# Kernel tuning notes

Measured on AMD Instinct MI355X. Metric: run time of the kernel, lower is better.

Reference implementation:

```python
import jax, jax.numpy as jnp
import numpy as np

K = 4  # recurrent_kernel_size


def setup_inputs() -> dict:
    key = jax.random.key(0)
    k1, k2, k3, k4 = jax.random.split(key, 4)
    b, t, d = 4, 4096, 1024
    x = jax.random.normal(k1, (b, t, d), dtype=jnp.float32)
    W_conv = jax.random.normal(k2, (d, 1, K), dtype=jnp.float32) * (1.0 / np.sqrt(K))
    W_proj = jax.random.normal(k3, (4 * d, d), dtype=jnp.float32) * (1.0 / np.sqrt(d))
    W_out = jax.random.normal(k4, (d, d), dtype=jnp.float32) * (1.0 / np.sqrt(d))
    return {"x": x, "W_conv": W_conv, "W_proj": W_proj, "W_out": W_out}


def _causal_dwconv(x_btd, W_conv):
    # x: [b,t,d]; W_conv: [d,1,k] (torch depthwise layout). Causal: left-pad k-1.
    d = x_btd.shape[-1]
    x_bdt = jnp.transpose(x_btd, (0, 2, 1))  # [b,d,t]
    y = jax.lax.conv_general_dilated(
        x_bdt, W_conv,
        window_strides=(1,),
        padding=[(K - 1, 0)],
        feature_group_count=d,
        dimension_numbers=("NCH", "OIH", "NCH"),
    )
    return jnp.transpose(y, (0, 2, 1))  # [b,t,d]


def reference(x, W_conv, W_proj, W_out):
    b, t, d = x.shape
    mixed = _causal_dwconv(x, W_conv)
    u = jnp.einsum("btd,ed->bte", x + mixed, W_proj)  # [b,t,4d]
    v, gate, decay, inject = jnp.split(u, 4, axis=-1)
    gate = jax.nn.sigmoid(gate)
    decay = jax.nn.sigmoid(decay)
    inject = jnp.tanh(inject)

    def step(state, inp):
        dec_t, inj_t, g_t, v_t = inp  # each [b,d]
        state = dec_t * state + (1.0 - dec_t) * inj_t
        out = g_t * v_t + (1.0 - g_t) * state
        return state, out

    # move time to leading axis for scan: [t,b,d]
    seq = (jnp.swapaxes(decay, 0, 1), jnp.swapaxes(inject, 0, 1),
           jnp.swapaxes(gate, 0, 1), jnp.swapaxes(v, 0, 1))
    state0 = jnp.zeros((b, d), dtype=x.dtype)
    _, y_tbd = jax.lax.scan(step, state0, seq)
    y = jnp.swapaxes(y_tbd, 0, 1)  # [b,t,d]
    return jnp.einsum("btd,ed->bte", y, W_out)
```

## Files before the change

kernel.cpp:

```cpp
#include <hip/hip_runtime.h>
#include <hip/hip_bf16.h>
#include <math.h>

typedef __hip_bfloat16 bf16;
typedef __bf16 bf16x8 __attribute__((ext_vector_type(8)));
typedef float f32x4 __attribute__((ext_vector_type(4)));
typedef float f32x4v __attribute__((ext_vector_type(4)));
typedef unsigned short u16x8v __attribute__((ext_vector_type(8)));
typedef unsigned short u16x4v __attribute__((ext_vector_type(4)));

#define BB 4
#define TT 4096
#define DD 1024

__device__ __forceinline__ float fast_sigmoid(float x) {
  return 1.0f / (1.0f + __expf(-x));
}
__device__ __forceinline__ float fast_tanh(float x) {
  return 2.0f / (1.0f + __expf(-2.0f * x)) - 1.0f;
}
__device__ __forceinline__ float b2f(unsigned short u) {
  union { unsigned int i; float f; } x;
  x.i = ((unsigned int)u) << 16;
  return x.f;
}
__device__ __forceinline__ unsigned short f2b(float f) {
  union { bf16 h; unsigned short u; } x;
  x.h = __float2bfloat16(f);
  return x.u;
}

__global__ __launch_bounds__(256) void w2bf_kernel(const float* __restrict__ w,
                                                   bf16* __restrict__ o,
                                                   int n) {
  int i = blockIdx.x * 256 + threadIdx.x;
  if (i < n) o[i] = __float2bfloat16(w[i]);
}

__global__ __launch_bounds__(256) void conv_add_kernel(
    const float* __restrict__ x, const float* __restrict__ Wc,
    bf16* __restrict__ xm, int total4) {
  int i = blockIdx.x * 256 + threadIdx.x;
  if (i >= total4) return;
  int c4 = (i & (DD / 4 - 1)) * 4;
  int t = (i / (DD / 4)) % TT;
  size_t base = (size_t)i * 4;
  f32x4v x0 = *(const f32x4v*)(x + base);
  f32x4v p1 = (t >= 1) ? *(const f32x4v*)(x + base - DD) : (f32x4v)0.0f;
  f32x4v p2 = (t >= 2) ? *(const f32x4v*)(x + base - 2 * DD) : (f32x4v)0.0f;
  f32x4v p3 = (t >= 3) ? *(const f32x4v*)(x + base - 3 * DD) : (f32x4v)0.0f;
  u16x4v o;
#pragma unroll
  for (int j = 0; j < 4; ++j) {
    f32x4v w = *(const f32x4v*)(Wc + (size_t)(c4 + j) * 4);
    float acc = x0[j] + w[3] * x0[j] + w[2] * p1[j] + w[1] * p2[j] +
                w[0] * p3[j];
    o[j] = f2b(acc);
  }
  *(u16x4v*)(xm + base) = o;
}

template <int EP>
__global__ __launch_bounds__(512, 2) void gemm256_kernel(
    const bf16* __restrict__ A, const bf16* __restrict__ B,
    void* __restrict__ C, int M, int N, int K, int MB) {
  __shared__ __align__(16) bf16 As[2][2][128][64];
  __shared__ __align__(16) bf16 Bs[2][2][128][64];

  const int tid = threadIdx.x;
  const int wv = tid >> 6, l = tid & 63;
  const int wm = wv >> 2, wn = wv & 3;

  const int bid = blockIdx.x;
  const int xcd = bid & 7, ii = bid >> 3;
  const int mb8 = MB >> 3;
  const int bm = xcd * mb8 + (ii % mb8);
  const int bn = ii / mb8;
  const int m0 = bm * 256, n0 = bn * 256;

  const int lr3 = l >> 3;
  const int gcolE = ((l & 7) ^ (l >> 3)) * 8;
  const int l15 = l & 15;
  const int rxor = (l15 & 7) << 3;
  const int lhi8 = (l >> 4) * 8;
  const int colK0 = lhi8 ^ rxor;
  const int colK1 = (32 + lhi8) ^ rxor;

  const char* AsB = (const char*)&As[0][0][0][0];
  const char* BsB = (const char*)&Bs[0][0][0][0];
  const int aB0 = wm * 16384 + l15 * 128 + colK0 * 2;
  const int aB1 = wm * 16384 + l15 * 128 + colK1 * 2;
  const int bB0 = (wn >> 1) * 16384 + (wn & 1) * 8192 + l15 * 128 + colK0 * 2;
  const int bB1 = (wn >> 1) * 16384 + (wn & 1) * 8192 + l15 * 128 + colK1 * 2;

  const bf16* Arow = A + (size_t)(m0 + wv * 16 + lr3) * K + gcolE;
  const bf16* Brow = B + (size_t)(n0 + wv * 16 + lr3) * K + gcolE;
  const bf16* ArowH = Arow + (size_t)128 * K;
  const bf16* BrowH = Brow + (size_t)128 * K;

  bf16* AsW = &As[0][0][0][0];
  bf16* BsW = &Bs[0][0][0][0];

  auto stage1 = [&](int which, int k0) {
    const int slot = (k0 >> 6) & 1;
    const bf16* src0 =
        (which == 0 ? Brow : which == 1 ? BrowH : which == 2 ? Arow : ArowH) +
        k0;
    bf16* dst0 = (which < 2 ? BsW : AsW) + slot * 16384 + (which & 1) * 8192 +
                 wv * 1024;
#pragma unroll
    for (int j = 0; j < 2; ++j) {
      __builtin_amdgcn_global_load_lds(
          (const __attribute__((address_space(1))) void*)(src0 +
                                                          (size_t)(j * 8) * K),
          (__attribute__((address_space(3))) void*)(dst0 + j * 512), 16, 0, 0);
    }
  };

  f32x4 acc[8][4];
#pragma unroll
  for (int i = 0; i < 8; ++i)
#pragma unroll
    for (int j = 0; j < 4; ++j) acc[i][j] = (f32x4)0.0f;

  const int NT2 = K >> 7;

  stage1(0, 0); stage1(1, 0); stage1(2, 0); stage1(3, 0);
  stage1(0, 64); stage1(1, 64); stage1(2, 64);
  asm volatile("s_waitcnt vmcnt(6)" ::: "memory");
  __builtin_amdgcn_s_barrier();

  bf16x8 aF[4][2], bF0[2][2], bF1[2][2];

  int kb = 0;
#pragma unroll 1
  for (int t = 0; t < NT2; ++t, kb += 128) {
#pragma unroll
    for (int g = 0; g < 8; ++g) {
      const int q = g & 3, grp = g >> 2;
      const int gof = grp * 32768;
      if (q == 0) {
#pragma unroll
        for (int mi = 0; mi < 4; ++mi) {
          aF[mi][0] = *(const bf16x8*)(AsB + aB0 + gof + mi * 2048);
          aF[mi][1] = *(const bf16x8*)(AsB + aB1 + gof + mi * 2048);
        }
#pragma unroll
        for (int ni = 0; ni < 2; ++ni) {
          bF0[ni][0] = *(const bf16x8*)(BsB + bB0 + gof + ni * 2048);
          bF0[ni][1] = *(const bf16x8*)(BsB + bB1 + gof + ni * 2048);
        }
      } else if (q == 1) {
#pragma unroll
        for (int ni = 0; ni < 2; ++ni) {
          bF1[ni][0] = *(const bf16x8*)(BsB + bB0 + gof + (ni + 2) * 2048);
          bF1[ni][1] = *(const bf16x8*)(BsB + bB1 + gof + (ni + 2) * 2048);
        }
      } else if (q == 2) {
#pragma unroll
        for (int mi = 0; mi < 4; ++mi) {
          aF[mi][0] = *(const bf16x8*)(AsB + aB0 + gof + (mi + 4) * 2048);
          aF[mi][1] = *(const bf16x8*)(AsB + aB1 + gof + (mi + 4) * 2048);
        }
      }
      if (t < NT2 - 1 || g == 0)
        stage1((7 + g) & 3, kb + 64 * ((7 + g) >> 2));
      __builtin_amdgcn_sched_barrier(0);
      __builtin_amdgcn_s_barrier();
      __builtin_amdgcn_s_setprio(1);
#pragma unroll
      for (int ks = 0; ks < 2; ++ks)
#pragma unroll
        for (int mi = 0; mi < 4; ++mi)
#pragma unroll
          for (int nj = 0; nj < 2; ++nj)
            acc[mi + (q >= 2 ? 4 : 0)][nj + ((q & 1) ? 2 : 0)] =
                __builtin_amdgcn_mfma_f32_16x16x32_bf16(
                    aF[mi][ks], (q & 1) ? bF1[nj][ks] : bF0[nj][ks],
                    acc[mi + (q >= 2 ? 4 : 0)][nj + ((q & 1) ? 2 : 0)], 0, 0,
                    0);
      __builtin_amdgcn_s_setprio(0);
      if (q == 3) {
        if (g == 3 && t == NT2 - 1)
          asm volatile("s_waitcnt vmcnt(0)" ::: "memory");
        else
          asm volatile("s_waitcnt vmcnt(6)" ::: "memory");
        __builtin_amdgcn_sched_barrier(0);
      }
      __builtin_amdgcn_s_barrier();
    }
  }

#pragma unroll
  for (int mi = 0; mi < 8; ++mi) {
    const int row = m0 + wm * 128 + mi * 16 + (l >> 4) * 4;
#pragma unroll
    for (int ni = 0; ni < 4; ++ni) {
      const int col = n0 + wn * 64 + ni * 16 + l15;
#pragma unroll
      for (int j = 0; j < 4; ++j) {
        float v = acc[mi][ni][j];
        if (EP == 0) {
          ((float*)C)[(size_t)(row + j) * N + col] = v;
        } else {
          const int cls = col >> 10;
          if (cls == 1 || cls == 2) v = fast_sigmoid(v);
          else if (cls == 3) v = fast_tanh(v);
          ((bf16*)C)[(size_t)(row + j) * N + col] = __float2bfloat16(v);
        }
      }
    }
  }
}

#define BM 64
#define BN 64
#define BKK 16
__global__ __launch_bounds__(256) void gemm_nt_kernel(
    const bf16* __restrict__ A, const float* __restrict__ B,
    float* __restrict__ C, int M, int N, int K) {
  __shared__ float Asm[BKK][BM + 1];
  __shared__ float Bsm[BKK][BN + 1];
  const int n0 = blockIdx.x * BN;
  const int m0 = blockIdx.y * BM;
  const int tid = threadIdx.x;
  const int tx = tid & 15, ty = tid >> 4;
  const int lk = tid & 15, lr = tid >> 4;
  float acc[4][4] = {};
  for (int k0 = 0; k0 < K; k0 += BKK) {
#pragma unroll
    for (int p = 0; p < 4; ++p) {
      Asm[lk][lr + 16 * p] =
          __bfloat162float(A[(size_t)(m0 + lr + 16 * p) * K + (k0 + lk)]);
      Bsm[lk][lr + 16 * p] = B[(size_t)(n0 + lr + 16 * p) * K + (k0 + lk)];
    }
    __syncthreads();
#pragma unroll
    for (int kk = 0; kk < BKK; ++kk) {
      float a[4], b[4];
#pragma unroll
      for (int i = 0; i < 4; ++i) a[i] = Asm[kk][ty * 4 + i];
#pragma unroll
      for (int j = 0; j < 4; ++j) b[j] = Bsm[kk][tx * 4 + j];
#pragma unroll
      for (int i = 0; i < 4; ++i)
#pragma unroll
        for (int j = 0; j < 4; ++j) acc[i][j] += a[i] * b[j];
    }
    __syncthreads();
  }
#pragma unroll
  for (int i = 0; i < 4; ++i)
#pragma unroll
    for (int j = 0; j < 4; ++j)
      C[(size_t)(m0 + ty * 4 + i) * N + (n0 + tx * 4 + j)] = acc[i][j];
}

__global__ __launch_bounds__(256) void scan_chunk_kernel(
    const bf16* __restrict__ u, float* __restrict__ cA,
    float* __restrict__ cB, int nchunk, int tchunk) {
  int idx = blockIdx.x * 256 + threadIdx.x;
  int c8 = (idx & (DD / 8 - 1)) * 8;
  int chunk = (idx / (DD / 8)) % nchunk;
  int b = idx / ((DD / 8) * nchunk);
  const bf16* ub = u + (size_t)b * TT * 4 * DD;
  float Aacc[8], Bacc[8];
#pragma unroll
  for (int j = 0; j < 8; ++j) { Aacc[j] = 1.0f; Bacc[j] = 0.0f; }
  int t0 = chunk * tchunk;
  for (int t = t0; t < t0 + tchunk; ++t) {
    const bf16* row = ub + (size_t)t * 4 * DD;
    u16x8v dv = *(const u16x8v*)(row + 2 * DD + c8);
    u16x8v iv = *(const u16x8v*)(row + 3 * DD + c8);
#pragma unroll
    for (int j = 0; j < 8; ++j) {
      float dec = b2f(dv[j]), inj = b2f(iv[j]);
      Aacc[j] *= dec;
      Bacc[j] = dec * Bacc[j] + (1.0f - dec) * inj;
    }
  }
  int base = (b * nchunk + chunk) * DD + c8;
#pragma unroll
  for (int j = 0; j < 8; ++j) { cA[base + j] = Aacc[j]; cB[base + j] = Bacc[j]; }
}

__global__ __launch_bounds__(256) void scan_prefix_kernel(
    const float* __restrict__ cA, const float* __restrict__ cB,
    float* __restrict__ S, int nchunk) {
  int idx = blockIdx.x * 256 + threadIdx.x;
  int c = idx % DD;
  int b = idx / DD;
  float s = 0.0f;
  for (int j = 0; j < nchunk; ++j) {
    int e = (b * nchunk + j) * DD + c;
    S[e] = s;
    s = cA[e] * s + cB[e];
  }
}

__global__ __launch_bounds__(256) void scan_out_kernel(
    const bf16* __restrict__ u, const float* __restrict__ S,
    bf16* __restrict__ y, int nchunk, int tchunk) {
  int idx = blockIdx.x * 256 + threadIdx.x;
  int c8 = (idx & (DD / 8 - 1)) * 8;
  int chunk = (idx / (DD / 8)) % nchunk;
  int b = idx / ((DD / 8) * nchunk);
  const bf16* ub = u + (size_t)b * TT * 4 * DD;
  bf16* yb = y + (size_t)b * TT * DD;
  float st[8];
  int sbase = (b * nchunk + chunk) * DD + c8;
#pragma unroll
  for (int j = 0; j < 8; ++j) st[j] = S[sbase + j];
  int t0 = chunk * tchunk;
  for (int t = t0; t < t0 + tchunk; ++t) {
    const bf16* row = ub + (size_t)t * 4 * DD;
    u16x8v vv = *(const u16x8v*)(row + c8);
    u16x8v gv = *(const u16x8v*)(row + DD + c8);
    u16x8v dv = *(const u16x8v*)(row + 2 * DD + c8);
    u16x8v iv = *(const u16x8v*)(row + 3 * DD + c8);
    u16x8v ov;
#pragma unroll
    for (int j = 0; j < 8; ++j) {
      float dec = b2f(dv[j]), inj = b2f(iv[j]);
      float g = b2f(gv[j]), v = b2f(vv[j]);
      st[j] = dec * st[j] + (1.0f - dec) * inj;
      ov[j] = f2b(g * v + (1.0f - g) * st[j]);
    }
    *(u16x8v*)(yb + (size_t)t * DD + c8) = ov;
  }
}

extern "C" void kernel_launch(void* const* d_in, const int* in_sizes, int n_in,
                              void* d_out, int out_size, void* d_ws,
                              size_t ws_size, hipStream_t stream) {
  const float* x = (const float*)d_in[0];
  const float* Wc = (const float*)d_in[1];
  const float* Wp = (const float*)d_in[2];
  const float* Wo = (const float*)d_in[3];
  float* out = (float*)d_out;

  const size_t nb = (size_t)TT * DD;

  auto need = [&](int nbat, int nchunk, bool wob) -> size_t {
    return (size_t)nbat * nb * 2 + (size_t)nbat * 4 * nb * 2 +
           (size_t)4 * DD * DD * 2 + (wob ? (size_t)DD * DD * 2 : 0) +
           (size_t)3 * nbat * nchunk * DD * 4;
  };

  int nbat, nchunk;
  bool haveWob;
  if (ws_size >= need(4, 64, true)) {
    nbat = 4; nchunk = 64; haveWob = true;
  } else if (ws_size >= need(1, 64, true)) {
    nbat = 1; nchunk = 64; haveWob = true;
  } else {
    nbat = 1; nchunk = 16; haveWob = false;
  }
  const int tchunk = TT / nchunk;

  char* p = (char*)d_ws;
  bf16* Wpb = (bf16*)p;  p += (size_t)4 * DD * DD * 2;
  bf16* Wob = nullptr;
  if (haveWob) { Wob = (bf16*)p; p += (size_t)DD * DD * 2; }
  bf16* xm = (bf16*)p;   p += (size_t)nbat * nb * 2;
  bf16* u = (bf16*)p;    p += (size_t)nbat * 4 * nb * 2;
  float* cA = (float*)p; p += (size_t)nbat * nchunk * DD * 4;
  float* cB = (float*)p; p += (size_t)nbat * nchunk * DD * 4;
  float* S = (float*)p;
  bf16* y = xm;

  w2bf_kernel<<<(4 * DD * DD) / 256, 256, 0, stream>>>(Wp, Wpb, 4 * DD * DD);
  if (haveWob)
    w2bf_kernel<<<(DD * DD) / 256, 256, 0, stream>>>(Wo, Wob, DD * DD);

  for (int b0 = 0; b0 < BB; b0 += nbat) {
    const float* xb = x + (size_t)b0 * nb;
    float* outb = out + (size_t)b0 * nb;
    const int Mtot = nbat * TT;
    const int total4 = (int)(nbat * nb / 4);

    conv_add_kernel<<<total4 / 256, 256, 0, stream>>>(xb, Wc, xm, total4);

    {
      const int MB = Mtot / 256;
      const int nwg = MB * (4 * DD / 256);
      gemm256_kernel<1><<<nwg, 512, 0, stream>>>(xm, Wpb, u, Mtot, 4 * DD, DD,
                                                 MB);
    }
    {
      int nthreads = nbat * nchunk * (DD / 8);
      scan_chunk_kernel<<<nthreads / 256, 256, 0, stream>>>(u, cA, cB, nchunk,
                                                            tchunk);
      scan_prefix_kernel<<<(nbat * DD) / 256, 256, 0, stream>>>(cA, cB, S,
                                                                nchunk);
      scan_out_kernel<<<nthreads / 256, 256, 0, stream>>>(u, S, y, nchunk,
                                                          tchunk);
    }
    if (haveWob) {
      const int MB = Mtot / 256;
      const int nwg = MB * (DD / 256);
      gemm256_kernel<0><<<nwg, 512, 0, stream>>>(y, Wob, outb, Mtot, DD, DD,
                                                 MB);
    } else {
      dim3 grid(DD / BN, Mtot / BM);
      gemm_nt_kernel<<<grid, 256, 0, stream>>>(y, Wo, outb, Mtot, DD, DD);
    }
  }
}
```

Baseline: 315.7 us.

## Replace 256x256 GEMM tile with a 128x128 double-buffered BK=32 kernel

```diff
diff --git a/kernel.cpp b/kernel.cpp
--- a/kernel.cpp
+++ b/kernel.cpp
@@ -8,6 +8,9 @@
 typedef float f32x4v __attribute__((ext_vector_type(4)));
 typedef unsigned short u16x8v __attribute__((ext_vector_type(8)));
 typedef unsigned short u16x4v __attribute__((ext_vector_type(4)));
+
+#define AS1 __attribute__((address_space(1)))
+#define AS3 __attribute__((address_space(3)))
 
 #define BB 4
 #define TT 4096
@@ -61,145 +64,106 @@
 }
 
 template <int EP>
-__global__ __launch_bounds__(512, 2) void gemm256_kernel(
+__global__ __launch_bounds__(256, 4) void gemm128_kernel(
     const bf16* __restrict__ A, const bf16* __restrict__ B,
     void* __restrict__ C, int M, int N, int K, int MB) {
-  __shared__ __align__(16) bf16 As[2][2][128][64];
-  __shared__ __align__(16) bf16 Bs[2][2][128][64];
+  __shared__ __align__(16) bf16 As[2][128][32];
+  __shared__ __align__(16) bf16 Bs[2][128][32];
 
   const int tid = threadIdx.x;
   const int wv = tid >> 6, l = tid & 63;
-  const int wm = wv >> 2, wn = wv & 3;
+  const int wm = wv >> 1, wn = wv & 1;
 
   const int bid = blockIdx.x;
   const int xcd = bid & 7, ii = bid >> 3;
   const int mb8 = MB >> 3;
   const int bm = xcd * mb8 + (ii % mb8);
   const int bn = ii / mb8;
-  const int m0 = bm * 256, n0 = bn * 256;
-
-  const int lr3 = l >> 3;
-  const int gcolE = ((l & 7) ^ (l >> 3)) * 8;
+  const int m0 = bm * 128, n0 = bn * 128;
+
+  const int srow = l >> 2;
+  const int scolE = ((l & 3) ^ ((l >> 2) & 3)) * 8;
+  const bf16* Ab = A + (size_t)(m0 + wv * 32 + srow) * K + scolE;
+  const bf16* Bb = B + (size_t)(n0 + wv * 32 + srow) * K + scolE;
+
   const int l15 = l & 15;
-  const int rxor = (l15 & 7) << 3;
-  const int lhi8 = (l >> 4) * 8;
-  const int colK0 = lhi8 ^ rxor;
-  const int colK1 = (32 + lhi8) ^ rxor;
-
-  const char* AsB = (const char*)&As[0][0][0][0];
-  const char* BsB = (const char*)&Bs[0][0][0][0];
-  const int aB0 = wm * 16384 + l15 * 128 + colK0 * 2;
-  const int aB1 = wm * 16384 + l15 * 128 + colK1 * 2;
-  const int bB0 = (wn >> 1) * 16384 + (wn & 1) * 8192 + l15 * 128 + colK0 * 2;
-  const int bB1 = (wn >> 1) * 16384 + (wn & 1) * 8192 + l15 * 128 + colK1 * 2;
-
-  const bf16* Arow = A + (size_t)(m0 + wv * 16 + lr3) * K + gcolE;
-  const bf16* Brow = B + (size_t)(n0 + wv * 16 + lr3) * K + gcolE;
-  const bf16* ArowH = Arow + (size_t)128 * K;
-  const bf16* BrowH = Brow + (size_t)128 * K;
-
-  bf16* AsW = &As[0][0][0][0];
-  bf16* BsW = &Bs[0][0][0][0];
-
-  auto stage1 = [&](int which, int k0) {
-    const int slot = (k0 >> 6) & 1;
-    const bf16* src0 =
-        (which == 0 ? Brow : which == 1 ? BrowH : which == 2 ? Arow : ArowH) +
-        k0;
-    bf16* dst0 = (which < 2 ? BsW : AsW) + slot * 16384 + (which & 1) * 8192 +
-                 wv * 1024;
+  const int physColB = ((l >> 4) ^ (l & 3)) * 16;
+  const char* AsB = (const char*)As;
+  const char* BsB = (const char*)Bs;
+  const int aBase = wm * 4096 + l15 * 64 + physColB;
+  const int bBase = wn * 4096 + l15 * 64 + physColB;
+
+  auto stageKt = [&](int kt, int slot) {
+    const int k0 = kt * 32;
 #pragma unroll
     for (int j = 0; j < 2; ++j) {
       __builtin_amdgcn_global_load_lds(
-          (const __attribute__((address_space(1))) void*)(src0 +
-                                                          (size_t)(j * 8) * K),
-          (__attribute__((address_space(3))) void*)(dst0 + j * 512), 16, 0, 0);
+          (const AS1 void*)(Ab + (size_t)(j * 16) * K + k0),
+          (AS3 void*)&As[slot][wv * 32 + j * 16][0], 16, 0, 0);
+      __builtin_amdgcn_global_load_lds(
+          (const AS1 void*)(Bb + (size_t)(j * 16) * K + k0),
+          (AS3 void*)&Bs[slot][wv * 32 + j * 16][0], 16, 0, 0);
     }
   };
 
-  f32x4 acc[8][4];
-#pragma unroll
-  for (int i = 0; i < 8; ++i)
+  f32x4 acc[4][4];
+#pragma unroll
+  for (int i = 0; i < 4; ++i)
 #pragma unroll
     for (int j = 0; j < 4; ++j) acc[i][j] = (f32x4)0.0f;
 
-  const int NT2 = K >> 7;
-
-  stage1(0, 0); stage1(1, 0); stage1(2, 0); stage1(3, 0);
-  stage1(0, 64); stage1(1, 64); stage1(2, 64);
-  asm volatile("s_waitcnt vmcnt(6)" ::: "memory");
+  const int NT = K >> 5;
+
+  stageKt(0, 0);
+  stageKt(1, 1);
+  asm volatile("s_waitcnt vmcnt(4)" ::: "memory");
   __builtin_amdgcn_s_barrier();
 
-  bf16x8 aF[4][2], bF0[2][2], bF1[2][2];
-
-  int kb = 0;
+  bf16x8 aF[4], bF[4];
+
 #pragma unroll 1
-  for (int t = 0; t < NT2; ++t, kb += 128) {
-#pragma unroll
-    for (int g = 0; g < 8; ++g) {
-      const int q = g & 3, grp = g >> 2;
-      const int gof = grp * 32768;
-      if (q == 0) {
-#pragma unroll
-        for (int mi = 0; mi < 4; ++mi) {
-          aF[mi][0] = *(const bf16x8*)(AsB + aB0 + gof + mi * 2048);
-          aF[mi][1] = *(const bf16x8*)(AsB + aB1 + gof + mi * 2048);
-        }
-#pragma unroll
-        for (int ni = 0; ni < 2; ++ni) {
-          bF0[ni][0] = *(const bf16x8*)(BsB + bB0 + gof + ni * 2048);
-          bF0[ni][1] = *(const bf16x8*)(BsB + bB1 + gof + ni * 2048);
-        }
-      } else if (q == 1) {
-#pragma unroll
-        for (int ni = 0; ni < 2; ++ni) {
-          bF1[ni][0] = *(const bf16x8*)(BsB + bB0 + gof + (ni + 2) * 2048);
-          bF1[ni][1] = *(const bf16x8*)(BsB + bB1 + gof + (ni + 2) * 2048);
-        }
-      } else if (q == 2) {
-#pragma unroll
-        for (int mi = 0; mi < 4; ++mi) {
-          aF[mi][0] = *(const bf16x8*)(AsB + aB0 + gof + (mi + 4) * 2048);
-          aF[mi][1] = *(const bf16x8*)(AsB + aB1 + gof + (mi + 4) * 2048);
-        }
-      }
-      if (t < NT2 - 1 || g == 0)
-        stage1((7 + g) & 3, kb + 64 * ((7 + g) >> 2));
+  for (int t = 0; t < NT / 2; ++t) {
+#pragma unroll
+    for (int s = 0; s < 2; ++s) {
+      const int kt = 2 * t + s;
+      const int sof = s * 8192;
+#pragma unroll
+      for (int mi = 0; mi < 4; ++mi)
+        aF[mi] = *(const bf16x8*)(AsB + aBase + sof + mi * 1024);
+#pragma unroll
+      for (int nj = 0; nj < 4; ++nj)
+        bF[nj] = *(const bf16x8*)(BsB + bBase + sof + nj * 1024);
       __builtin_amdgcn_sched_barrier(0);
       __builtin_amdgcn_s_barrier();
       __builtin_amdgcn_s_setprio(1);
 #pragma unroll
-      for (int ks = 0; ks < 2; ++ks)
-#pragma unroll
-        for (int mi = 0; mi < 4; ++mi)
-#pragma unroll
-          for (int nj = 0; nj < 2; ++nj)
-            acc[mi + (q >= 2 ? 4 : 0)][nj + ((q & 1) ? 2 : 0)] =
-                __builtin_amdgcn_mfma_f32_16x16x32_bf16(
-                    aF[mi][ks], (q & 1) ? bF1[nj][ks] : bF0[nj][ks],
-                    acc[mi + (q >= 2 ? 4 : 0)][nj + ((q & 1) ? 2 : 0)], 0, 0,
-                    0);
+      for (int mi = 0; mi < 4; ++mi)
+#pragma unroll
+        for (int nj = 0; nj < 4; ++nj)
+          acc[mi][nj] = __builtin_amdgcn_mfma_f32_16x16x32_bf16(
+              aF[mi], bF[nj], acc[mi][nj], 0, 0, 0);
       __builtin_amdgcn_s_setprio(0);
-      if (q == 3) {
-        if (g == 3 && t == NT2 - 1)
+      if (kt + 2 < NT) stageKt(kt + 2, s);
+      if (kt + 1 < NT) {
+        if (kt + 2 < NT)
+          asm volatile("s_waitcnt vmcnt(4)" ::: "memory");
+        else
           asm volatile("s_waitcnt vmcnt(0)" ::: "memory");
-        else
-          asm volatile("s_waitcnt vmcnt(6)" ::: "memory");
-        __builtin_amdgcn_sched_barrier(0);
       }
+      __builtin_amdgcn_sched_barrier(0);
       __builtin_amdgcn_s_barrier();
     }
   }
 
 #pragma unroll
-  for (int mi = 0; mi < 8; ++mi) {
-    const int row = m0 + wm * 128 + mi * 16 + (l >> 4) * 4;
-#pragma unroll
-    for (int ni = 0; ni < 4; ++ni) {
-      const int col = n0 + wn * 64 + ni * 16 + l15;
+  for (int mi = 0; mi < 4; ++mi) {
+    const int row = m0 + wm * 64 + mi * 16 + (l >> 4) * 4;
+#pragma unroll
+    for (int nj = 0; nj < 4; ++nj) {
+      const int col = n0 + wn * 64 + nj * 16 + l15;
 #pragma unroll
       for (int j = 0; j < 4; ++j) {
-        float v = acc[mi][ni][j];
+        float v = acc[mi][nj][j];
         if (EP == 0) {
           ((float*)C)[(size_t)(row + j) * N + col] = v;
         } else {
@@ -382,9 +346,9 @@
     conv_add_kernel<<<total4 / 256, 256, 0, stream>>>(xb, Wc, xm, total4);
 
     {
-      const int MB = Mtot / 256;
-      const int nwg = MB * (4 * DD / 256);
-      gemm256_kernel<1><<<nwg, 512, 0, stream>>>(xm, Wpb, u, Mtot, 4 * DD, DD,
+      const int MB = Mtot / 128;
+      const int nwg = MB * (4 * DD / 128);
+      gemm128_kernel<1><<<nwg, 256, 0, stream>>>(xm, Wpb, u, Mtot, 4 * DD, DD,
                                                  MB);
     }
     {
@@ -397,9 +361,9 @@
                                                           tchunk);
     }
     if (haveWob) {
-      const int MB = Mtot / 256;
-      const int nwg = MB * (DD / 256);
-      gemm256_kernel<0><<<nwg, 512, 0, stream>>>(y, Wob, outb, Mtot, DD, DD,
+      const int MB = Mtot / 128;
+      const int nwg = MB * (DD / 128);
+      gemm128_kernel<0><<<nwg, 256, 0, stream>>>(y, Wob, outb, Mtot, DD, DD,
                                                  MB);
     } else {
       dim3 grid(DD / BN, Mtot / BM);
```

Measured after the change: 342.2 us. 8.4% more time.

## Add 128x128 tile GEMM for projection and remap 256 GEMM workgroup order

Applied to the files above, without the earlier changes.

```diff
diff --git a/kernel.cpp b/kernel.cpp
--- a/kernel.cpp
+++ b/kernel.cpp
@@ -8,6 +8,9 @@
 typedef float f32x4v __attribute__((ext_vector_type(4)));
 typedef unsigned short u16x8v __attribute__((ext_vector_type(8)));
 typedef unsigned short u16x4v __attribute__((ext_vector_type(4)));
+
+#define AS1 __attribute__((address_space(1)))
+#define AS3 __attribute__((address_space(3)))
 
 #define BB 4
 #define TT 4096
@@ -61,6 +64,120 @@
 }
 
 template <int EP>
+__global__ __launch_bounds__(256, 4) void gemm128_kernel(
+    const bf16* __restrict__ A, const bf16* __restrict__ B,
+    void* __restrict__ C, int M, int N, int K, int MB) {
+  __shared__ __align__(16) bf16 As[2][128][32];
+  __shared__ __align__(16) bf16 Bs[2][128][32];
+
+  const int tid = threadIdx.x;
+  const int wv = tid >> 6, l = tid & 63;
+  const int wm = wv >> 1, wn = wv & 1;
+
+  const int bid = blockIdx.x;
+  const int xcd = bid & 7, ii = bid >> 3;
+  const int mb8 = MB >> 3;
+  const int bm = xcd * mb8 + (ii % mb8);
+  const int bn = ii / mb8;
+  const int m0 = bm * 128, n0 = bn * 128;
+
+  const int srow = l >> 2;
+  const int scolE = ((l & 3) ^ ((l >> 3) & 3)) * 8;
+  const bf16* Ab = A + (size_t)(m0 + wv * 32 + srow) * K + scolE;
+  const bf16* Bb = B + (size_t)(n0 + wv * 32 + srow) * K + scolE;
+
+  const int l15 = l & 15;
+  const int physColB = ((l >> 4) ^ ((l >> 1) & 3)) * 16;
+  const char* AsB = (const char*)As;
+  const char* BsB = (const char*)Bs;
+  const int aBase = wm * 4096 + l15 * 64 + physColB;
+  const int bBase = wn * 4096 + l15 * 64 + physColB;
+
+  auto stageKt = [&](int kt, int slot) {
+    const int k0 = kt * 32;
+#pragma unroll
+    for (int j = 0; j < 2; ++j) {
+      __builtin_amdgcn_global_load_lds(
+          (const AS1 void*)(Ab + (size_t)(j * 16) * K + k0),
+          (AS3 void*)&As[slot][wv * 32 + j * 16][0], 16, 0, 0);
+      __builtin_amdgcn_global_load_lds(
+          (const AS1 void*)(Bb + (size_t)(j * 16) * K + k0),
+          (AS3 void*)&Bs[slot][wv * 32 + j * 16][0], 16, 0, 0);
+    }
+  };
+
+  f32x4 acc[4][4];
+#pragma unroll
+  for (int i = 0; i < 4; ++i)
+#pragma unroll
+    for (int j = 0; j < 4; ++j) acc[i][j] = (f32x4)0.0f;
+
+  const int NT = K >> 5;
+
+  stageKt(0, 0);
+  stageKt(1, 1);
+  asm volatile("s_waitcnt vmcnt(4)" ::: "memory");
+  __builtin_amdgcn_s_barrier();
+
+  bf16x8 aF[4], bF[4];
+
+#pragma unroll 1
+  for (int t = 0; t < NT / 2; ++t) {
+#pragma unroll
+    for (int s = 0; s < 2; ++s) {
+      const int kt = 2 * t + s;
+      const int sof = s * 8192;
+#pragma unroll
+      for (int mi = 0; mi < 4; ++mi)
+        aF[mi] = *(const bf16x8*)(AsB + aBase + sof + mi * 1024);
+#pragma unroll
+      for (int nj = 0; nj < 4; ++nj)
+        bF[nj] = *(const bf16x8*)(BsB + bBase + sof + nj * 1024);
+      __builtin_amdgcn_sched_barrier(0);
+      __builtin_amdgcn_s_barrier();
+      __builtin_amdgcn_s_setprio(1);
+#pragma unroll
+      for (int mi = 0; mi < 4; ++mi)
+#pragma unroll
+        for (int nj = 0; nj < 4; ++nj)
+          acc[mi][nj] = __builtin_amdgcn_mfma_f32_16x16x32_bf16(
+              aF[mi], bF[nj], acc[mi][nj], 0, 0, 0);
+      __builtin_amdgcn_s_setprio(0);
+      if (kt + 2 < NT) stageKt(kt + 2, s);
+      if (kt + 1 < NT) {
+        if (kt + 2 < NT)
+          asm volatile("s_waitcnt vmcnt(4)" ::: "memory");
+        else
+          asm volatile("s_waitcnt vmcnt(0)" ::: "memory");
+      }
+      __builtin_amdgcn_sched_barrier(0);
+      __builtin_amdgcn_s_barrier();
+    }
+  }
+
+#pragma unroll
+  for (int mi = 0; mi < 4; ++mi) {
+    const int row = m0 + wm * 64 + mi * 16 + (l >> 4) * 4;
+#pragma unroll
+    for (int nj = 0; nj < 4; ++nj) {
+      const int col = n0 + wn * 64 + nj * 16 + l15;
+#pragma unroll
+      for (int j = 0; j < 4; ++j) {
+        float v = acc[mi][nj][j];
+        if (EP == 0) {
+          ((float*)C)[(size_t)(row + j) * N + col] = v;
+        } else {
+          const int cls = col >> 10;
+          if (cls == 1 || cls == 2) v = fast_sigmoid(v);
+          else if (cls == 3) v = fast_tanh(v);
+          ((bf16*)C)[(size_t)(row + j) * N + col] = __float2bfloat16(v);
+        }
+      }
+    }
+  }
+}
+
+template <int EP>
 __global__ __launch_bounds__(512, 2) void gemm256_kernel(
     const bf16* __restrict__ A, const bf16* __restrict__ B,
     void* __restrict__ C, int M, int N, int K, int MB) {
@@ -71,11 +188,11 @@
   const int wv = tid >> 6, l = tid & 63;
   const int wm = wv >> 2, wn = wv & 3;
 
+  const int nwg = gridDim.x;
+  const int cpx = nwg >> 3;
   const int bid = blockIdx.x;
-  const int xcd = bid & 7, ii = bid >> 3;
-  const int mb8 = MB >> 3;
-  const int bm = xcd * mb8 + (ii % mb8);
-  const int bn = ii / mb8;
+  const int wg = (bid & 7) * cpx + (bid >> 3);
+  const int bm = wg % MB, bn = wg / MB;
   const int m0 = bm * 256, n0 = bn * 256;
 
   const int lr3 = l >> 3;
@@ -111,9 +228,8 @@
 #pragma unroll
     for (int j = 0; j < 2; ++j) {
       __builtin_amdgcn_global_load_lds(
-          (const __attribute__((address_space(1))) void*)(src0 +
-                                                          (size_t)(j * 8) * K),
-          (__attribute__((address_space(3))) void*)(dst0 + j * 512), 16, 0, 0);
+          (const AS1 void*)(src0 + (size_t)(j * 8) * K),
+          (AS3 void*)(dst0 + j * 512), 16, 0, 0);
     }
   };
 
@@ -382,9 +498,9 @@
     conv_add_kernel<<<total4 / 256, 256, 0, stream>>>(xb, Wc, xm, total4);
 
     {
-      const int MB = Mtot / 256;
-      const int nwg = MB * (4 * DD / 256);
-      gemm256_kernel<1><<<nwg, 512, 0, stream>>>(xm, Wpb, u, Mtot, 4 * DD, DD,
+      const int MB = Mtot / 128;
+      const int nwg = MB * (4 * DD / 128);
+      gemm128_kernel<1><<<nwg, 256, 0, stream>>>(xm, Wpb, u, Mtot, 4 * DD, DD,
                                                  MB);
     }
     {
```

Result: slower. 336.7 us (+6.7%).
